# Performance work log

Measured on AMD Instinct MI355X. Metric: run time of the kernel, lower is better.

Reference implementation:

```python
import jax, jax.numpy as jnp
import numpy as np

D = 512
H = 4
HD = D // H
FF = 4 * D
B = 512
T = 128
EMA_K = 128
LOC_K = 4
DECAY = 0.9
STEP = 0.5 / np.sqrt(128 / 32)  # 0.25
EPS = 1e-5


def layernorm(x, g, b):
    mu = jnp.mean(x, axis=-1, keepdims=True)
    var = jnp.mean(jnp.square(x - mu), axis=-1, keepdims=True)
    return (x - mu) * jax.lax.rsqrt(var + EPS) * g + b


def dwconv_causal(x, w):
    # x: (B,T,D), w: (D,K); torch Conv1d(groups=D, padding=K-1) sliced to [:T]
    K = w.shape[1]
    xt = jnp.transpose(x, (0, 2, 1))  # (B,D,T)
    y = jax.lax.conv_general_dilated(
        xt, w[:, None, :], window_strides=(1,), padding=[(K - 1, 0)],
        feature_group_count=x.shape[-1], dimension_numbers=('NCT', 'OIT', 'NCT'))
    return jnp.transpose(y, (0, 2, 1))


def rope(qk, cos, sin):
    # qk: (B,H,T,HD)
    x1, x2 = jnp.split(qk, 2, axis=-1)
    rot = jnp.concatenate([-x2, x1], axis=-1)
    return qk * cos + rot * sin


def setup_inputs() -> dict:
    key = jax.random.key(0)
    ks = jax.random.split(key, 24)
    s = 0.02
    inp = {
        'parallel_repr': jax.random.normal(ks[0], (B, T, D), jnp.float32),
        'sequential_state': jax.random.normal(ks[1], (B, D), jnp.float32),
        'q_w': jax.random.normal(ks[2], (D, D), jnp.float32) * s,
        'q_b': jnp.zeros((D,), jnp.float32),
        'k_w': jax.random.normal(ks[3], (D, D), jnp.float32) * s,
        'k_b': jnp.zeros((D,), jnp.float32),
        'v_w': jax.random.normal(ks[4], (D, D), jnp.float32) * s,
        'v_b': jnp.zeros((D,), jnp.float32),
        'o_w': jax.random.normal(ks[5], (D, D), jnp.float32) * s,
        'o_b': jnp.zeros((D,), jnp.float32),
        'local_w': jax.random.normal(ks[6], (D, LOC_K), jnp.float32) * 0.1,
        'local_b': jax.random.normal(ks[7], (D,), jnp.float32) * 0.1,
        'delta_w': jax.random.normal(ks[8], (3 * D, D), jnp.float32) * s,
        'delta_b': jnp.zeros((D,), jnp.float32),
        'gate_w': jax.random.normal(ks[9], (3 * D, D), jnp.float32) * s,
        'gate_b': jnp.zeros((D,), jnp.float32),
        'dn_g': jnp.ones((D,), jnp.float32), 'dn_b': jnp.zeros((D,), jnp.float32),
        'ln1_g': jnp.ones((D,), jnp.float32), 'ln1_b': jnp.zeros((D,), jnp.float32),
        'ln2_g': jnp.ones((D,), jnp.float32), 'ln2_b': jnp.zeros((D,), jnp.float32),
        'ln3_g': jnp.ones((D,), jnp.float32), 'ln3_b': jnp.zeros((D,), jnp.float32),
        'ln4_g': jnp.ones((D,), jnp.float32), 'ln4_b': jnp.zeros((D,), jnp.float32),
        'seq_w': jax.random.normal(ks[10], (D, D), jnp.float32) * s,
        'seq_b': jnp.zeros((D,), jnp.float32),
        'ffn_w1': jax.random.normal(ks[11], (D, FF), jnp.float32) * s,
        'ffn_b1': jnp.zeros((FF,), jnp.float32),
        'ffn_w2': jax.random.normal(ks[12], (FF, D), jnp.float32) * s,
        'ffn_b2': jnp.zeros((D,), jnp.float32),
    }
    # EMA kernel: coefficient (1-d)*d^lag on x[t-lag]; stored flipped as in torch
    ema = (1.0 - DECAY) * DECAY ** jnp.arange(EMA_K, dtype=jnp.float32)
    inp['ema_w'] = jnp.broadcast_to(ema[::-1][None, :], (D, EMA_K))
    return inp


def reference(parallel_repr, sequential_state, q_w, q_b, k_w, k_b, v_w, v_b,
              o_w, o_b, local_w, local_b, delta_w, delta_b, gate_w, gate_b,
              dn_g, dn_b, ln1_g, ln1_b, ln2_g, ln2_b, ln3_g, ln3_b, ln4_g, ln4_b,
              seq_w, seq_b, ffn_w1, ffn_b1, ffn_w2, ffn_b2, ema_w):
    x = parallel_repr
    Bb, Tt, Dd = x.shape
    # --- RoPE causal attention ---
    inv_freq = 1.0 / (10000.0 ** (jnp.arange(0, HD, 2, dtype=jnp.float32) / HD))
    t = jnp.arange(Tt, dtype=jnp.float32)
    freqs = jnp.outer(t, inv_freq)                      # (T, HD/2)
    emb = jnp.concatenate([freqs, freqs], axis=-1)      # (T, HD)
    cos = jnp.cos(emb)[None, None]
    sin = jnp.sin(emb)[None, None]
    def heads(y):
        return jnp.transpose(y.reshape(Bb, Tt, H, HD), (0, 2, 1, 3))
    q = rope(heads(x @ q_w + q_b), cos, sin)
    k = rope(heads(x @ k_w + k_b), cos, sin)
    v = heads(x @ v_w + v_b)
    scores = jnp.einsum('bhtd,bhsd->bhts', q, k) / np.sqrt(HD)
    causal = jnp.tril(jnp.ones((Tt, Tt), dtype=bool))
    scores = jnp.where(causal, scores, jnp.float32(-1e9))
    attn = jax.nn.softmax(scores, axis=-1)
    attn_out = jnp.einsum('bhts,bhsd->bhtd', attn, v)
    attn_out = jnp.transpose(attn_out, (0, 2, 1, 3)).reshape(Bb, Tt, Dd)
    attn_out = attn_out @ o_w + o_b
    x1 = layernorm(x + attn_out, ln1_g, ln1_b)
    # --- depthwise causal convs ---
    local_hist = dwconv_causal(x1, local_w) + local_b
    global_sum = dwconv_causal(x1, ema_w)
    combined = jnp.concatenate([x1, local_hist, global_sum], axis=-1)  # (B,T,3D)
    deltas = jax.nn.sigmoid(combined @ gate_w + gate_b) * jnp.tanh(combined @ delta_w + delta_b)
    deltas = layernorm(deltas, dn_g, dn_b)
    acc = jnp.cumsum(deltas, axis=1) * STEP
    states = layernorm(sequential_state[:, None, :] + acc, ln3_g, ln3_b)
    seq_guidance = states @ seq_w + seq_b
    ffn_in = x1 + 0.3 * seq_guidance
    h = jax.nn.gelu(ffn_in @ ffn_w1 + ffn_b1, approximate=False)
    ffn_out = h @ ffn_w2 + ffn_b2
    out = layernorm(x1 + ffn_out, ln2_g, ln2_b)
    final_state = layernorm(states[:, -1, :], ln4_g, ln4_b)
    return out, final_state
```

## Files before the change

kernel.cpp:

```cpp
#include <hip/hip_runtime.h>
#include <cstddef>
#include <cstdint>

#define BB   512
#define TT   128
#define DD   512
#define HH   4
#define HDIM 128
#define FFD  2048
#define NROWS (BB * TT)
#define SLOT ((size_t)NROWS * DD)

typedef unsigned short u16;
typedef __bf16 bf16x8 __attribute__((ext_vector_type(8)));
typedef float  f32x4  __attribute__((ext_vector_type(4)));

__device__ __forceinline__ u16 f2b(float x) {
    union { float f; unsigned u; } v; v.f = x;
    unsigned r = v.u + 0x7FFFu + ((v.u >> 16) & 1u);
    return (u16)(r >> 16);
}
__device__ __forceinline__ float b2f(u16 u) {
    union { unsigned u; float f; } v; v.u = (unsigned)u << 16; return v.f;
}
__device__ __forceinline__ float fast_gelu(float v) {
    float t = v * (0.7978845608028654f + 0.0356774081f * v * v);
    float e = __expf(2.f * t);
    float th = 1.f - 2.f / (e + 1.f);
    return 0.5f * v * (1.f + th);
}
__device__ __forceinline__ void glds16(const void* g, void* l) {
    __builtin_amdgcn_global_load_lds(
        (const __attribute__((address_space(1))) void*)g,
        (__attribute__((address_space(3))) void*)l, 16, 0, 0);
}

#define PH_BAR() do { __builtin_amdgcn_sched_barrier(0); \
                      __builtin_amdgcn_s_barrier(); \
                      __builtin_amdgcn_sched_barrier(0); } while (0)

template<int MODE>
__global__ __launch_bounds__(512, 2)
void gemm256(const u16* __restrict__ A, const u16* __restrict__ BT,
             const float* __restrict__ bias, void* __restrict__ Cout, int ldc,
             const float* __restrict__ addsrc, int K, int M)
{
    __shared__ u16 S[65536];
    const int tid = threadIdx.x;
    const int gx  = gridDim.x;
    const int nwg = gx * gridDim.y;
    int orig = blockIdx.y * gx + blockIdx.x;
    orig = (orig & 7) * (nwg >> 3) + (orig >> 3);
    const int row0 = (orig / gx) * 256;
    const int col0 = (orig % gx) * 256;

    const int lane = tid & 63;
    const int wid  = tid >> 6;
    const int wm   = wid >> 2;
    const int wn   = wid & 3;
    const int fr   = lane & 15;
    const int kq   = lane >> 4;

    const int c0 = wid * 128 + lane;
    const int c1 = c0 + 64;
    const int l0 = c0 ^ (((c0 >> 5) & 1) << 1);
    const int l1 = c1 ^ (((c1 >> 5) & 1) << 1);
    const int sr0 = l0 >> 2, sk0 = (l0 & 3) * 8;
    const int sr1 = l1 >> 2, sk1 = (l1 & 3) * 8;
    const u16* ApG = A  + (size_t)row0 * K;
    const u16* BpG = BT + (size_t)col0 * K;

    auto stA = [&](int kt, int kh) {
        char* slot = (char*)S + ((((kt & 1) << 1) + kh) << 14);
        const u16* g = ApG + kt * 64 + kh * 32;
        glds16(g + (size_t)sr0 * K + sk0, slot + c0 * 16);
        glds16(g + (size_t)sr1 * K + sk1, slot + c1 * 16);
    };
    auto stB = [&](int kt, int kh) {
        char* slot = (char*)S + 65536 + ((((kt & 1) << 1) + kh) << 14);
        const u16* g = BpG + kt * 64 + kh * 32;
        glds16(g + (size_t)sr0 * K + sk0, slot + c0 * 16);
        glds16(g + (size_t)sr1 * K + sk1, slot + c1 * 16);
    };
    auto rdA = [&](int p, int kh, int m) -> bf16x8 {
        const int row = wm * 128 + m * 16 + fr;
        const int L = (row * 64 + kq * 16) ^ (((row >> 3) & 1) << 5);
        return *(const bf16x8*)((char*)S + (((p << 1) + kh) << 14) + L);
    };
    auto rdB = [&](int p, int kh, int n) -> bf16x8 {
        const int col = wn * 64 + n * 16 + fr;
        const int L = (col * 64 + kq * 16) ^ (((col >> 3) & 1) << 5);
        return *(const bf16x8*)((char*)S + 65536 + (((p << 1) + kh) << 14) + L);
    };

    f32x4 acc[8][4];
#pragma unroll
    for (int m = 0; m < 8; ++m)
#pragma unroll
        for (int n = 0; n < 4; ++n) acc[m][n] = (f32x4){0.f, 0.f, 0.f, 0.f};

    const int NKT = K >> 6;

    stA(0, 0); stA(0, 1); stB(0, 0); stB(0, 1);
    stB(1, 0); stA(1, 0); stB(1, 1);
    asm volatile("s_waitcnt vmcnt(6)" ::: "memory");
    __builtin_amdgcn_s_barrier();

    bf16x8 b0, b1, b2, b3;
#define MFMA16(MH, A0, A1, A2, A3)                                              \
    do {                                                                        \
        __builtin_amdgcn_s_setprio(1);                                          \
        bf16x8 aa_[4] = {A0, A1, A2, A3};                                       \
        bf16x8 bb_[4] = {b0, b1, b2, b3};                                       \
        _Pragma("unroll")                                                       \
        for (int m_ = 0; m_ < 4; ++m_)                                          \
            _Pragma("unroll")                                                   \
            for (int n_ = 0; n_ < 4; ++n_)                                      \
                acc[(MH) * 4 + m_][n_] = __builtin_amdgcn_mfma_f32_16x16x32_bf16( \
                    aa_[m_], bb_[n_], acc[(MH) * 4 + m_][n_], 0, 0, 0);         \
        __builtin_amdgcn_s_setprio(0);                                          \
    } while (0)

    for (int kt = 0; kt < NKT; ++kt) {
        const int p = kt & 1;
        const bool s1 = (kt + 1 < NKT);
        const bool s2 = (kt + 2 < NKT);
        {
            bf16x8 a0 = rdA(p, 0, 0), a1 = rdA(p, 0, 1), a2 = rdA(p, 0, 2), a3 = rdA(p, 0, 3);
            b0 = rdB(p, 0, 0); b1 = rdB(p, 0, 1); b2 = rdB(p, 0, 2); b3 = rdB(p, 0, 3);
            if (s1) stA(kt + 1, 1);
            PH_BAR();
            MFMA16(0, a0, a1, a2, a3);
            PH_BAR();
        }
        {
            bf16x8 a0 = rdA(p, 0, 4), a1 = rdA(p, 0, 5), a2 = rdA(p, 0, 6), a3 = rdA(p, 0, 7);
            if (s2) stB(kt + 2, 0);
            PH_BAR();
            MFMA16(1, a0, a1, a2, a3);
            PH_BAR();
        }
        {
            bf16x8 a0 = rdA(p, 1, 0), a1 = rdA(p, 1, 1), a2 = rdA(p, 1, 2), a3 = rdA(p, 1, 3);
            b0 = rdB(p, 1, 0); b1 = rdB(p, 1, 1); b2 = rdB(p, 1, 2); b3 = rdB(p, 1, 3);
            if (s2) stA(kt + 2, 0);
            PH_BAR();
            MFMA16(0, a0, a1, a2, a3);
            PH_BAR();
        }
        {
            bf16x8 a0 = rdA(p, 1, 4), a1 = rdA(p, 1, 5), a2 = rdA(p, 1, 6), a3 = rdA(p, 1, 7);
            if (s2) stB(kt + 2, 1);
            PH_BAR();
            MFMA16(1, a0, a1, a2, a3);
            if (s2)      asm volatile("s_waitcnt vmcnt(6)" ::: "memory");
            else if (s1) asm volatile("s_waitcnt vmcnt(0)" ::: "memory");
            PH_BAR();
        }
    }
#undef MFMA16

#pragma unroll
    for (int m = 0; m < 8; ++m) {
#pragma unroll
        for (int jj = 0; jj < 4; ++jj) {
            const int r = row0 + wm * 128 + m * 16 + kq * 4 + jj;
#pragma unroll
            for (int n = 0; n < 4; ++n) {
                const int c = col0 + wn * 64 + n * 16 + fr;
                float v = acc[m][n][jj] + bias[c];
                if constexpr (MODE == 2) {
                    ((u16*)Cout)[(size_t)r * ldc + c] =
                        f2b(addsrc[(size_t)r * M + c] + 0.3f * v);
                } else if constexpr (MODE == 3) {
                    ((u16*)Cout)[(size_t)r * ldc + c] = f2b(fast_gelu(v));
                } else if constexpr (MODE == 6) {
                    float pth = __shfl_xor(v, 1);
                    if ((fr & 1) == 0) {
                        float sg = 1.f / (1.f + __expf(-v));
                        float e  = __expf(2.f * pth);
                        float th = 1.f - 2.f / (e + 1.f);
                        ((u16*)Cout)[(size_t)r * ldc + (c >> 1)] = f2b(sg * th);
                    }
                } else {
                    ((u16*)Cout)[(size_t)r * ldc + c] = f2b(v);
                }
            }
        }
    }
}

template<int MODE>
__global__ __launch_bounds__(256)
void gemm_bf16(const u16* __restrict__ A, const u16* __restrict__ BT,
               const float* __restrict__ bias, void* __restrict__ Cout, int ldc,
               const float* __restrict__ addsrc, void* __restrict__ aux,
               int K, int M)
{
    __shared__ u16 smem[16384];
    const int tid = threadIdx.x;
    const int gx  = gridDim.x;
    const int nwg = gx * gridDim.y;
    int orig = blockIdx.y * gx + blockIdx.x;
    if ((nwg & 7) == 0) orig = (orig & 7) * (nwg >> 3) + (orig >> 3);
    const int row0 = (orig / gx) * 128;
    const int col0 = (orig % gx) * 128;

    const int lane = tid & 63;
    const int w    = tid >> 6;
    const int wr   = (w >> 1) * 64;
    const int wc   = (w & 1) * 64;
    const int fr   = lane & 15;
    const int kg   = (lane >> 4) * 8;

    f32x4 acc[4][4];
#pragma unroll
    for (int m = 0; m < 4; ++m)
#pragma unroll
        for (int n = 0; n < 4; ++n) acc[m][n] = (f32x4){0.f, 0.f, 0.f, 0.f};

    const int srow = tid >> 2;
    const int skb  = (tid & 3) * 8;
    const u16* Ag = A  + (size_t)(row0 + srow) * K + skb;
    const u16* Bg = BT + (size_t)(col0 + srow) * K + skb;
    const int soff = srow * 32 + skb;

    auto stage = [&](int kt, int buf) {
        const int ko = kt * 32;
        u16* as = smem + buf * 8192 + soff;
        u16* bs = smem + buf * 8192 + 4096 + soff;
        glds16(Ag + ko,                  as);
        glds16(Ag + (size_t)64 * K + ko, as + 2048);
        glds16(Bg + ko,                  bs);
        glds16(Bg + (size_t)64 * K + ko, bs + 2048);
    };

    const int nk = K >> 5;
    stage(0, 0);
    for (int k = 0; k < nk; ++k) {
        if (k + 1 < nk) {
            stage(k + 1, (k + 1) & 1);
            asm volatile("s_waitcnt vmcnt(4)" ::: "memory");
        } else {
            asm volatile("s_waitcnt vmcnt(0)" ::: "memory");
        }
        __syncthreads();
        const u16* As = smem + (k & 1) * 8192;
        const u16* Bs = As + 4096;
        bf16x8 af[4], bfr[4];
#pragma unroll
        for (int m = 0; m < 4; ++m)
            af[m] = *reinterpret_cast<const bf16x8*>(&As[(wr + m * 16 + fr) * 32 + kg]);
#pragma unroll
        for (int n = 0; n < 4; ++n)
            bfr[n] = *reinterpret_cast<const bf16x8*>(&Bs[(wc + n * 16 + fr) * 32 + kg]);
#pragma unroll
        for (int m = 0; m < 4; ++m)
#pragma unroll
            for (int n = 0; n < 4; ++n)
                acc[m][n] = __builtin_amdgcn_mfma_f32_16x16x32_bf16(af[m], bfr[n], acc[m][n], 0, 0, 0);
        __syncthreads();
    }

    if constexpr (MODE == 7) {
        if (col0 >= 1024) {
#pragma unroll
            for (int m = 0; m < 4; ++m)
#pragma unroll
                for (int j = 0; j < 4; ++j) {
                    const int tl = wr + m * 16 + (lane >> 4) * 4 + j;
#pragma unroll
                    for (int n = 0; n < 4; ++n) {
                        const int dc = wc + n * 16 + fr;
                        float v = acc[m][n][j] + bias[col0 + dc];
                        *(u16*)((char*)smem + dc * 256 + ((tl * 2) ^ ((dc & 7) << 4))) = f2b(v);
                    }
                }
            __syncthreads();
            u16* dst = (u16*)aux + ((size_t)((row0 >> 7) * 4 + ((col0 - 1024) >> 7)) << 14);
#pragma unroll
            for (int i = 0; i < 8; ++i)
                *(uint4*)(dst + (size_t)(i * 256 + tid) * 8) =
                    *(const uint4*)((char*)smem + (size_t)(i * 256 + tid) * 16);
        } else {
#pragma unroll
            for (int m = 0; m < 4; ++m)
#pragma unroll
                for (int j = 0; j < 4; ++j) {
                    const int r = row0 + wr + m * 16 + (lane >> 4) * 4 + j;
#pragma unroll
                    for (int n = 0; n < 4; ++n) {
                        const int c = col0 + wc + n * 16 + fr;
                        ((u16*)Cout)[(size_t)r * 1024 + c] = f2b(acc[m][n][j] + bias[c]);
                    }
                }
        }
    }
    (void)ldc; (void)addsrc;
}

__global__ __launch_bounds__(256)
void wtrans_kernel(const float* __restrict__ W, u16* __restrict__ WT, int K, int M,
                   int rmul, int roff)
{
    __shared__ float t[32][33];
    const int m0 = blockIdx.x * 32;
    const int k0 = blockIdx.y * 32;
    const int tx = threadIdx.x;
    const int ty = threadIdx.y;
#pragma unroll
    for (int i = 0; i < 4; ++i) {
        int k = ty * 4 + i;
        t[k][tx] = W[(size_t)(k0 + k) * M + m0 + tx];
    }
    __syncthreads();
#pragma unroll
    for (int i = 0; i < 4; ++i) {
        int m = ty * 4 + i;
        WT[(size_t)((m0 + m) * rmul + roff) * K + k0 + tx] = f2b(t[tx][m]);
    }
}

__global__ void cast_f2b_kernel(const float* __restrict__ in, u16* __restrict__ out, size_t n4)
{
    size_t i = (size_t)blockIdx.x * blockDim.x + threadIdx.x;
    if (i >= n4) return;
    float4 v = reinterpret_cast<const float4*>(in)[i];
    union { u16 u[4]; uint2 d; } p;
    p.u[0] = f2b(v.x); p.u[1] = f2b(v.y); p.u[2] = f2b(v.z); p.u[3] = f2b(v.w);
    reinterpret_cast<uint2*>(out)[i] = p.d;
}

__global__ void rope_table_kernel(float* __restrict__ tabc, float* __restrict__ tabs)
{
    int idx = blockIdx.x * blockDim.x + threadIdx.x;
    if (idx >= TT * 64) return;
    int t = idx >> 6, j = idx & 63;
    float invf = expf(-(float)j * (9.210340371976184f / 64.f));
    float ang  = (float)t * invf;
    tabc[idx] = cosf(ang);
    tabs[idx] = sinf(ang);
}

__global__ void bias_build_kernel(const float* qb, const float* kb, const float* vb,
                                  const float* gb, const float* db,
                                  float* qkvb, float* gdb)
{
    int i = blockIdx.x * blockDim.x + threadIdx.x;
    if (i >= 512) return;
    qkvb[i] = qb[i]; qkvb[512 + i] = kb[i]; qkvb[1024 + i] = vb[i];
    gdb[2 * i] = gb[i]; gdb[2 * i + 1] = db[i];
}

__global__ __launch_bounds__(256)
void attn_mfma_kernel(const u16* __restrict__ QKg, const u16* __restrict__ VTg,
                      u16* __restrict__ Og,
                      const float* __restrict__ tabc, const float* __restrict__ tabs)
{
    __shared__ u16 SA[128 * 128];
    __shared__ u16 SB[128 * 128];
    const int h = blockIdx.x, b = blockIdx.y;
    const int tid  = threadIdx.x;
    const int lane = tid & 63;
    const int w    = tid >> 6;
    const int fr   = lane & 15;
    const int kq   = lane >> 4;
    const size_t baseq = ((size_t)(b * TT)) * 1024 + (size_t)h * HDIM;
    const size_t baseo = ((size_t)(b * TT)) * DD + (size_t)h * HDIM;

    {
        const int tg = tid >> 4;
        const int dg = tid & 15;
        const int j0 = (dg & 7) * 8;
        const bool hi = (dg & 8) != 0;
        for (int r = 0; r < 8; ++r) {
            const int t = r * 16 + tg;
            uint4 qv = *(const uint4*)(QKg + baseq + (size_t)t * 1024 + dg * 8);
            uint4 kv = *(const uint4*)(QKg + baseq + 512 + (size_t)t * 1024 + dg * 8);
            unsigned qa[4] = {qv.x, qv.y, qv.z, qv.w};
            unsigned ka[4] = {kv.x, kv.y, kv.z, kv.w};
            unsigned qb[4], kb[4];
#pragma unroll
            for (int i = 0; i < 4; ++i) {
                qb[i] = __shfl_xor((int)qa[i], 8);
                kb[i] = __shfl_xor((int)ka[i], 8);
            }
            const float* cp = tabc + t * 64 + j0;
            const float* sp = tabs + t * 64 + j0;
            u16 oq[8], ok[8];
#pragma unroll
            for (int e = 0; e < 8; ++e) {
                float fq = b2f((u16)(qa[e >> 1] >> ((e & 1) * 16)));
                float gq = b2f((u16)(qb[e >> 1] >> ((e & 1) * 16)));
                float fk = b2f((u16)(ka[e >> 1] >> ((e & 1) * 16)));
                float gk = b2f((u16)(kb[e >> 1] >> ((e & 1) * 16)));
                float c = cp[e], s = sp[e];
                oq[e] = f2b(hi ? fq * c + gq * s : fq * c - gq * s);
                ok[e] = f2b(hi ? fk * c + gk * s : fk * c - gk * s);
            }
            const int cb = (dg * 16) ^ ((t & 7) << 4);
            *(uint4*)((char*)SA + t * 256 + cb) = *(const uint4*)oq;
            *(uint4*)((char*)SB + t * 256 + cb) = *(const uint4*)ok;
        }
    }
    __syncthreads();

    f32x4 acc[2][8];
#pragma unroll
    for (int m = 0; m < 2; ++m)
#pragma unroll
        for (int n = 0; n < 8; ++n) acc[m][n] = (f32x4){0.f, 0.f, 0.f, 0.f};

    for (int k0 = 0; k0 < 128; k0 += 32) {
        const int cb = (k0 + kq * 8) * 2;
        bf16x8 af[2];
#pragma unroll
        for (int m = 0; m < 2; ++m) {
            const int row = w * 32 + m * 16 + fr;
            af[m] = *(const bf16x8*)((char*)SA + row * 256 + (cb ^ ((row & 7) << 4)));
        }
#pragma unroll
        for (int n = 0; n < 8; ++n) {
            const int row = n * 16 + fr;
            bf16x8 bf = *(const bf16x8*)((char*)SB + row * 256 + (cb ^ ((row & 7) << 4)));
            acc[0][n] = __builtin_amdgcn_mfma_f32_16x16x32_bf16(af[0], bf, acc[0][n], 0, 0, 0);
            acc[1][n] = __builtin_amdgcn_mfma_f32_16x16x32_bf16(af[1], bf, acc[1][n], 0, 0, 0);
        }
    }
    __syncthreads();

    {
        const u16* vsrc = VTg + ((size_t)(b * HH + h) << 14);
#pragma unroll
        for (int i = 0; i < 8; ++i)
            glds16(vsrc + (size_t)(i * 256 + tid) * 8,
                   SB + (size_t)(i * 256 + tid) * 8);
    }

    const float SC = 0.08838834764831845f;
#pragma unroll
    for (int m = 0; m < 2; ++m) {
#pragma unroll
        for (int j = 0; j < 4; ++j) {
            const int t = w * 32 + m * 16 + kq * 4 + j;
            float mx = -3.0e38f;
#pragma unroll
            for (int n = 0; n < 8; ++n) {
                const int s = n * 16 + fr;
                float v = acc[m][n][j];
                v = (s <= t) ? v * SC : -3.0e38f;
                acc[m][n][j] = v;
                mx = fmaxf(mx, v);
            }
            mx = fmaxf(mx, __shfl_xor(mx, 1));
            mx = fmaxf(mx, __shfl_xor(mx, 2));
            mx = fmaxf(mx, __shfl_xor(mx, 4));
            mx = fmaxf(mx, __shfl_xor(mx, 8));
            float sum = 0.f;
#pragma unroll
            for (int n = 0; n < 8; ++n) {
                float e = __expf(acc[m][n][j] - mx);
                acc[m][n][j] = e; sum += e;
            }
            sum += __shfl_xor(sum, 1); sum += __shfl_xor(sum, 2);
            sum += __shfl_xor(sum, 4); sum += __shfl_xor(sum, 8);
            const float inv = 1.f / sum;
#pragma unroll
            for (int n = 0; n < 8; ++n) {
                const int s = n * 16 + fr;
                *(u16*)((char*)SA + t * 256 + ((s * 2) ^ ((t & 7) << 4))) =
                    f2b(acc[m][n][j] * inv);
            }
        }
    }
    __syncthreads();

    f32x4 oa[2][8];
#pragma unroll
    for (int m = 0; m < 2; ++m)
#pragma unroll
        for (int n = 0; n < 8; ++n) oa[m][n] = (f32x4){0.f, 0.f, 0.f, 0.f};

    for (int k0 = 0; k0 < 128; k0 += 32) {
        const int cb = (k0 + kq * 8) * 2;
        bf16x8 pa[2];
#pragma unroll
        for (int m = 0; m < 2; ++m) {
            const int row = w * 32 + m * 16 + fr;
            pa[m] = *(const bf16x8*)((char*)SA + row * 256 + (cb ^ ((row & 7) << 4)));
        }
#pragma unroll
        for (int n = 0; n < 8; ++n) {
            const int row = n * 16 + fr;
            bf16x8 vb = *(const bf16x8*)((char*)SB + row * 256 + (cb ^ ((row & 7) << 4)));
            oa[0][n] = __builtin_amdgcn_mfma_f32_16x16x32_bf16(pa[0], vb, oa[0][n], 0, 0, 0);
            oa[1][n] = __builtin_amdgcn_mfma_f32_16x16x32_bf16(pa[1], vb, oa[1][n], 0, 0, 0);
        }
    }

#pragma unroll
    for (int m = 0; m < 2; ++m)
#pragma unroll
        for (int j = 0; j < 4; ++j) {
            const int t = w * 32 + m * 16 + kq * 4 + j;
            u16* orow = Og + baseo + (size_t)t * DD;
#pragma unroll
            for (int n = 0; n < 8; ++n)
                orow[n * 16 + fr] = f2b(oa[m][j * 0 + n][j] * 0.f + oa[m][n][j]);
        }
}

__device__ __forceinline__ float2 blk_red512(float v, float (*red)[2], int tid)
{
    float s = v, ss = v * v;
#pragma unroll
    for (int off = 1; off < 64; off <<= 1) {
        s  += __shfl_xor(s, off);
        ss += __shfl_xor(ss, off);
    }
    if ((tid & 63) == 0) { red[tid >> 6][0] = s; red[tid >> 6][1] = ss; }
    __syncthreads();
    float S = 0.f, SS = 0.f;
#pragma unroll
    for (int w = 0; w < 8; ++w) { S += red[w][0]; SS += red[w][1]; }
    return make_float2(S, SS);
}

__global__ __launch_bounds__(512)
void ln1_chain_kernel(const float* __restrict__ x, const u16* __restrict__ oo,
                      const float* __restrict__ g, const float* __restrict__ bb,
                      const float* __restrict__ lw, const float* __restrict__ lb,
                      float* __restrict__ X1, u16* __restrict__ Cb)
{
    __shared__ float red[2][8][2];
    const int b = blockIdx.x, d = threadIdx.x;
    const float g_ = g[d], b_ = bb[d];
    const float w0 = lw[d * 4 + 0], w1 = lw[d * 4 + 1],
                w2 = lw[d * 4 + 2], w3 = lw[d * 4 + 3];
    const float lb_ = lb[d];
    const size_t rb = (size_t)b * TT;
    float h1 = 0.f, h2 = 0.f, h3 = 0.f, ema = 0.f;
    float v = x[(rb + 0) * DD + d] + b2f(oo[(rb + 0) * DD + d]);
    for (int t = 0; t < TT; ++t) {
        const int tn = (t < TT - 1) ? t + 1 : t;
        float vn = x[(rb + tn) * DD + d] + b2f(oo[(rb + tn) * DD + d]);
        float2 r = blk_red512(v, red[t & 1], d);
        float mu  = r.x * (1.f / DD);
        float var = r.y * (1.f / DD) - mu * mu;
        float x1v = (v - mu) * rsqrtf(var + 1e-5f) * g_ + b_;
        const size_t row = rb + t;
        X1[row * DD + d] = x1v;
        u16* crow = Cb + row * 1536;
        crow[d] = f2b(x1v);
        crow[512 + d]  = f2b(lb_ + w3 * x1v + w2 * h1 + w1 * h2 + w0 * h3);
        ema = 0.9f * ema + 0.1f * x1v;
        crow[1024 + d] = f2b(ema);
        h3 = h2; h2 = h1; h1 = x1v;
        v = vn;
    }
}

__global__ __launch_bounds__(512)
void state_chain_kernel(const u16* __restrict__ deltasB, const float* __restrict__ seqst,
                        const float* __restrict__ dng, const float* __restrict__ dnb,
                        const float* __restrict__ g3, const float* __restrict__ b3,
                        const float* __restrict__ g4, const float* __restrict__ b4,
                        u16* __restrict__ statesb, float* __restrict__ fstate)
{
    __shared__ float red[2][8][2];
    const int b = blockIdx.x, d = threadIdx.x;
    const float gd_ = dng[d], bd_ = dnb[d], g3_ = g3[d], b3_ = b3[d];
    const float seq = seqst[(size_t)b * DD + d];
    const size_t rb = (size_t)b * TT;
    float cum = 0.f;
    float v = b2f(deltasB[(rb + 0) * DD + d]);
    for (int t = 0; t < TT; ++t) {
        const int tn = (t < TT - 1) ? t + 1 : t;
        float vn = b2f(deltasB[(rb + tn) * DD + d]);
        float2 r0 = blk_red512(v, red[0], d);
        float mu  = r0.x * (1.f / DD);
        float var = r0.y * (1.f / DD) - mu * mu;
        float nd  = (v - mu) * rsqrtf(var + 1e-5f) * gd_ + bd_;
        cum += nd;
        float sv = seq + cum * 0.25f;
        float2 r1 = blk_red512(sv, red[1], d);
        mu  = r1.x * (1.f / DD);
        var = r1.y * (1.f / DD) - mu * mu;
        float o = (sv - mu) * rsqrtf(var + 1e-5f) * g3_ + b3_;
        statesb[(rb + t) * DD + d] = f2b(o);
        if (t == TT - 1) {
            float2 r2 = blk_red512(o, red[0], d);
            float mu4  = r2.x * (1.f / DD);
            float var4 = r2.y * (1.f / DD) - mu4 * mu4;
            fstate[(size_t)b * DD + d] = (o - mu4) * rsqrtf(var4 + 1e-5f) * g4[d] + b4[d];
        }
        v = vn;
    }
}

__global__ __launch_bounds__(256)
void ln2_kernel(const float* __restrict__ a, const u16* __restrict__ badd,
                const float* __restrict__ g, const float* __restrict__ bb,
                float* __restrict__ out)
{
    const int row = blockIdx.x;
    const int tid = threadIdx.x;
    const float* ap = a + (size_t)row * DD;
    const u16*   bp = badd + (size_t)row * DD;
    float v0 = ap[tid]       + b2f(bp[tid]);
    float v1 = ap[tid + 256] + b2f(bp[tid + 256]);
    float s  = v0 + v1;
    float ss = v0 * v0 + v1 * v1;
#pragma unroll
    for (int off = 1; off < 64; off <<= 1) {
        s  += __shfl_xor(s, off);
        ss += __shfl_xor(ss, off);
    }
    __shared__ float sm1[4], sm2[4];
    const int wid = tid >> 6;
    if ((tid & 63) == 0) { sm1[wid] = s; sm2[wid] = ss; }
    __syncthreads();
    s  = sm1[0] + sm1[1] + sm1[2] + sm1[3];
    ss = sm2[0] + sm2[1] + sm2[2] + sm2[3];
    const float mu  = s * (1.f / DD);
    const float var = ss * (1.f / DD) - mu * mu;
    const float r   = rsqrtf(var + 1e-5f);
    float* op = out + (size_t)row * DD;
    op[tid]       = (v0 - mu) * r * g[tid]       + bb[tid];
    op[tid + 256] = (v1 - mu) * r * g[tid + 256] + bb[tid + 256];
}

extern "C" void kernel_launch(void* const* d_in, const int* in_sizes, int n_in,
                              void* d_out, int out_size, void* d_ws, size_t ws_size,
                              hipStream_t stream)
{
    const float* x       = (const float*)d_in[0];
    const float* seqst   = (const float*)d_in[1];
    const float* q_w     = (const float*)d_in[2];
    const float* q_b     = (const float*)d_in[3];
    const float* k_w     = (const float*)d_in[4];
    const float* k_b     = (const float*)d_in[5];
    const float* v_w     = (const float*)d_in[6];
    const float* v_b     = (const float*)d_in[7];
    const float* o_w     = (const float*)d_in[8];
    const float* o_b     = (const float*)d_in[9];
    const float* local_w = (const float*)d_in[10];
    const float* local_b = (const float*)d_in[11];
    const float* delta_w = (const float*)d_in[12];
    const float* delta_b = (const float*)d_in[13];
    const float* gate_w  = (const float*)d_in[14];
    const float* gate_b  = (const float*)d_in[15];
    const float* dn_g    = (const float*)d_in[16];
    const float* dn_b    = (const float*)d_in[17];
    const float* ln1_g   = (const float*)d_in[18];
    const float* ln1_b   = (const float*)d_in[19];
    const float* ln2_g   = (const float*)d_in[20];
    const float* ln2_b   = (const float*)d_in[21];
    const float* ln3_g   = (const float*)d_in[22];
    const float* ln3_b   = (const float*)d_in[23];
    const float* ln4_g   = (const float*)d_in[24];
    const float* ln4_b   = (const float*)d_in[25];
    const float* seq_w   = (const float*)d_in[26];
    const float* seq_b   = (const float*)d_in[27];
    const float* ffn_w1  = (const float*)d_in[28];
    const float* ffn_b1  = (const float*)d_in[29];
    const float* ffn_w2  = (const float*)d_in[30];
    const float* ffn_b2  = (const float*)d_in[31];
    (void)in_sizes; (void)n_in; (void)out_size; (void)ws_size;

    float* out = (float*)d_out;
    char*  ws  = (char*)d_ws;
    const size_t MB = (size_t)1 << 20;

    u16*   xb      = (u16*)(ws + 0);
    u16*   QKb     = (u16*)(ws + 64 * MB);
    u16*   VTb     = (u16*)(ws + 192 * MB);
    u16*   attnb   = (u16*)(ws + 256 * MB);
    u16*   Oob     = (u16*)(ws + 0);
    u16*   Cb      = (u16*)(ws + 64 * MB);
    u16*   deltasB = (u16*)(ws + 256 * MB);
    u16*   statesb = (u16*)(ws + 320 * MB);
    u16*   ffn_inb = (u16*)(ws + 0);
    u16*   hb      = (u16*)(ws + 64 * MB);
    u16*   Fob     = (u16*)(ws + 320 * MB);
    u16*   WSq  = (u16*)(ws + 448 * MB);
    u16*   WSo  = (u16*)(ws + 450 * MB);
    u16*   WSgd = (u16*)(ws + 451 * MB);
    u16*   WSs  = (u16*)(ws + 455 * MB);
    u16*   WSf1 = (u16*)(ws + 456 * MB);
    u16*   WSf2 = (u16*)(ws + 458 * MB);
    float* qkvb = (float*)(ws + 460 * MB);
    float* gdb  = (float*)(ws + 461 * MB);

    float* X1     = out;
    float* tabc   = out + SLOT;
    float* tabs   = tabc + TT * 64;
    float* fstate = out + SLOT;

    const size_t NE = (size_t)NROWS * DD;

    rope_table_kernel<<<(TT * 64 + 255) / 256, 256, 0, stream>>>(tabc, tabs);
    cast_f2b_kernel<<<(unsigned)((NE / 4 + 255) / 256), 256, 0, stream>>>(x, xb, NE / 4);
    bias_build_kernel<<<2, 256, 0, stream>>>(q_b, k_b, v_b, gate_b, delta_b, qkvb, gdb);
    auto wt = [&](const float* W, u16* WT, int K, int M, int rmul, int roff) {
        wtrans_kernel<<<dim3(M / 32, K / 32), dim3(32, 8), 0, stream>>>(W, WT, K, M, rmul, roff);
    };
    wt(q_w, WSq, DD, DD, 1, 0);
    wt(k_w, WSq + (size_t)512 * DD, DD, DD, 1, 0);
    wt(v_w, WSq + (size_t)1024 * DD, DD, DD, 1, 0);
    wt(o_w, WSo, DD, DD, 1, 0);
    wt(gate_w,  WSgd, 3 * DD, DD, 2, 0);
    wt(delta_w, WSgd, 3 * DD, DD, 2, 1);
    wt(seq_w, WSs, DD, DD, 1, 0);
    wt(ffn_w1, WSf1, DD, FFD, 1, 0);
    wt(ffn_w2, WSf2, FFD, DD, 1, 0);

    gemm_bf16<7><<<dim3(12, 512), 256, 0, stream>>>(
        xb, WSq, qkvb, QKb, 1024, nullptr, VTb, DD, 1536);

    attn_mfma_kernel<<<dim3(HH, BB), 256, 0, stream>>>(QKb, VTb, attnb, tabc, tabs);

    gemm256<4><<<dim3(2, 256), 512, 0, stream>>>(
        attnb, WSo, o_b, Oob, DD, nullptr, DD, DD);

    ln1_chain_kernel<<<BB, 512, 0, stream>>>(x, Oob, ln1_g, ln1_b, local_w, local_b, X1, Cb);

    gemm256<6><<<dim3(4, 256), 512, 0, stream>>>(
        Cb, WSgd, gdb, deltasB, DD, nullptr, 3 * DD, 1024);

    state_chain_kernel<<<BB, 512, 0, stream>>>(
        deltasB, seqst, dn_g, dn_b, ln3_g, ln3_b, ln4_g, ln4_b, statesb, fstate);

    gemm256<2><<<dim3(2, 256), 512, 0, stream>>>(
        statesb, WSs, seq_b, ffn_inb, DD, X1, DD, DD);

    gemm256<3><<<dim3(8, 256), 512, 0, stream>>>(
        ffn_inb, WSf1, ffn_b1, hb, FFD, nullptr, DD, FFD);
    gemm256<4><<<dim3(2, 256), 512, 0, stream>>>(
        hb, WSf2, ffn_b2, Fob, DD, nullptr, FFD, DD);

    ln2_kernel<<<NROWS, 256, 0, stream>>>(X1, Fob, ln2_g, ln2_b, out);
}
```

Baseline: 1.668 ms.

## Reschedule GEMM main loop into N-half phases with fewer scheduling barriers

After: 1.655 ms. About the same (-0.8%).

```diff
diff --git a/kernel.cpp b/kernel.cpp
--- a/kernel.cpp
+++ b/kernel.cpp
@@ -35,9 +35,9 @@
         (__attribute__((address_space(3))) void*)l, 16, 0, 0);
 }
 
-#define PH_BAR() do { __builtin_amdgcn_sched_barrier(0); \
-                      __builtin_amdgcn_s_barrier(); \
-                      __builtin_amdgcn_sched_barrier(0); } while (0)
+#define BAR() asm volatile("s_barrier" ::: "memory")
+#define MM(ACC, AV, BV) \
+    ACC = __builtin_amdgcn_mfma_f32_16x16x32_bf16(AV, BV, ACC, 0, 0, 0)
 
 template<int MODE>
 __global__ __launch_bounds__(512, 2)
@@ -102,63 +102,81 @@
     const int NKT = K >> 6;
 
     stA(0, 0); stA(0, 1); stB(0, 0); stB(0, 1);
-    stB(1, 0); stA(1, 0); stB(1, 1);
+    stB(1, 0); stB(1, 1); stA(1, 0);
     asm volatile("s_waitcnt vmcnt(6)" ::: "memory");
-    __builtin_amdgcn_s_barrier();
-
-    bf16x8 b0, b1, b2, b3;
-#define MFMA16(MH, A0, A1, A2, A3)                                              \
-    do {                                                                        \
-        __builtin_amdgcn_s_setprio(1);                                          \
-        bf16x8 aa_[4] = {A0, A1, A2, A3};                                       \
-        bf16x8 bb_[4] = {b0, b1, b2, b3};                                       \
-        _Pragma("unroll")                                                       \
-        for (int m_ = 0; m_ < 4; ++m_)                                          \
-            _Pragma("unroll")                                                   \
-            for (int n_ = 0; n_ < 4; ++n_)                                      \
-                acc[(MH) * 4 + m_][n_] = __builtin_amdgcn_mfma_f32_16x16x32_bf16( \
-                    aa_[m_], bb_[n_], acc[(MH) * 4 + m_][n_], 0, 0, 0);         \
-        __builtin_amdgcn_s_setprio(0);                                          \
-    } while (0)
+    BAR();
 
     for (int kt = 0; kt < NKT; ++kt) {
         const int p = kt & 1;
         const bool s1 = (kt + 1 < NKT);
         const bool s2 = (kt + 2 < NKT);
-        {
-            bf16x8 a0 = rdA(p, 0, 0), a1 = rdA(p, 0, 1), a2 = rdA(p, 0, 2), a3 = rdA(p, 0, 3);
-            b0 = rdB(p, 0, 0); b1 = rdB(p, 0, 1); b2 = rdB(p, 0, 2); b3 = rdB(p, 0, 3);
-            if (s1) stA(kt + 1, 1);
-            PH_BAR();
-            MFMA16(0, a0, a1, a2, a3);
-            PH_BAR();
-        }
-        {
-            bf16x8 a0 = rdA(p, 0, 4), a1 = rdA(p, 0, 5), a2 = rdA(p, 0, 6), a3 = rdA(p, 0, 7);
-            if (s2) stB(kt + 2, 0);
-            PH_BAR();
-            MFMA16(1, a0, a1, a2, a3);
-            PH_BAR();
-        }
-        {
-            bf16x8 a0 = rdA(p, 1, 0), a1 = rdA(p, 1, 1), a2 = rdA(p, 1, 2), a3 = rdA(p, 1, 3);
-            b0 = rdB(p, 1, 0); b1 = rdB(p, 1, 1); b2 = rdB(p, 1, 2); b3 = rdB(p, 1, 3);
-            if (s2) stA(kt + 2, 0);
-            PH_BAR();
-            MFMA16(0, a0, a1, a2, a3);
-            PH_BAR();
-        }
-        {
-            bf16x8 a0 = rdA(p, 1, 4), a1 = rdA(p, 1, 5), a2 = rdA(p, 1, 6), a3 = rdA(p, 1, 7);
-            if (s2) stB(kt + 2, 1);
-            PH_BAR();
-            MFMA16(1, a0, a1, a2, a3);
-            if (s2)      asm volatile("s_waitcnt vmcnt(6)" ::: "memory");
-            else if (s1) asm volatile("s_waitcnt vmcnt(0)" ::: "memory");
-            PH_BAR();
-        }
-    }
-#undef MFMA16
+        bf16x8 a0, a1, a2, a3, a4, a5, a6, a7;
+        bf16x8 b00, b01, b02, b03, b10, b11, b12, b13;
+
+        if (s1) stA(kt + 1, 1);
+        a0 = rdA(p, 0, 0); a1 = rdA(p, 0, 1); a2 = rdA(p, 0, 2); a3 = rdA(p, 0, 3);
+        a4 = rdA(p, 1, 0); a5 = rdA(p, 1, 1); a6 = rdA(p, 1, 2); a7 = rdA(p, 1, 3);
+        b00 = rdB(p, 0, 0); b01 = rdB(p, 0, 1);
+        b10 = rdB(p, 1, 0); b11 = rdB(p, 1, 1);
+        BAR();
+        __builtin_amdgcn_s_setprio(1);
+        MM(acc[0][0], a0, b00); MM(acc[0][1], a0, b01);
+        MM(acc[1][0], a1, b00); MM(acc[1][1], a1, b01);
+        MM(acc[2][0], a2, b00); MM(acc[2][1], a2, b01);
+        MM(acc[3][0], a3, b00); MM(acc[3][1], a3, b01);
+        MM(acc[0][0], a4, b10); MM(acc[0][1], a4, b11);
+        MM(acc[1][0], a5, b10); MM(acc[1][1], a5, b11);
+        MM(acc[2][0], a6, b10); MM(acc[2][1], a6, b11);
+        MM(acc[3][0], a7, b10); MM(acc[3][1], a7, b11);
+        __builtin_amdgcn_s_setprio(0);
+        BAR();
+
+        b02 = rdB(p, 0, 2); b03 = rdB(p, 0, 3);
+        b12 = rdB(p, 1, 2); b13 = rdB(p, 1, 3);
+        BAR();
+        __builtin_amdgcn_s_setprio(1);
+        MM(acc[0][2], a0, b02); MM(acc[0][3], a0, b03);
+        MM(acc[1][2], a1, b02); MM(acc[1][3], a1, b03);
+        MM(acc[2][2], a2, b02); MM(acc[2][3], a2, b03);
+        MM(acc[3][2], a3, b02); MM(acc[3][3], a3, b03);
+        MM(acc[0][2], a4, b12); MM(acc[0][3], a4, b13);
+        MM(acc[1][2], a5, b12); MM(acc[1][3], a5, b13);
+        MM(acc[2][2], a6, b12); MM(acc[2][3], a6, b13);
+        MM(acc[3][2], a7, b12); MM(acc[3][3], a7, b13);
+        __builtin_amdgcn_s_setprio(0);
+        BAR();
+
+        if (s2) stB(kt + 2, 0);
+        a0 = rdA(p, 0, 4); a1 = rdA(p, 0, 5); a2 = rdA(p, 0, 6); a3 = rdA(p, 0, 7);
+        a4 = rdA(p, 1, 4); a5 = rdA(p, 1, 5); a6 = rdA(p, 1, 6); a7 = rdA(p, 1, 7);
+        BAR();
+        __builtin_amdgcn_s_setprio(1);
+        MM(acc[4][0], a0, b00); MM(acc[4][1], a0, b01);
+        MM(acc[5][0], a1, b00); MM(acc[5][1], a1, b01);
+        MM(acc[6][0], a2, b00); MM(acc[6][1], a2, b01);
+        MM(acc[7][0], a3, b00); MM(acc[7][1], a3, b01);
+        MM(acc[4][0], a4, b10); MM(acc[4][1], a4, b11);
+        MM(acc[5][0], a5, b10); MM(acc[5][1], a5, b11);
+        MM(acc[6][0], a6, b10); MM(acc[6][1], a6, b11);
+        MM(acc[7][0], a7, b10); MM(acc[7][1], a7, b11);
+        __builtin_amdgcn_s_setprio(0);
+        BAR();
+
+        if (s2) { stB(kt + 2, 1); stA(kt + 2, 0); }
+        __builtin_amdgcn_s_setprio(1);
+        MM(acc[4][2], a0, b02); MM(acc[4][3], a0, b03);
+        MM(acc[5][2], a1, b02); MM(acc[5][3], a1, b03);
+        MM(acc[6][2], a2, b02); MM(acc[6][3], a2, b03);
+        MM(acc[7][2], a3, b02); MM(acc[7][3], a3, b03);
+        MM(acc[4][2], a4, b12); MM(acc[4][3], a4, b13);
+        MM(acc[5][2], a5, b12); MM(acc[5][3], a5, b13);
+        MM(acc[6][2], a6, b12); MM(acc[6][3], a6, b13);
+        MM(acc[7][2], a7, b12); MM(acc[7][3], a7, b13);
+        __builtin_amdgcn_s_setprio(0);
+        if (s2)      asm volatile("s_waitcnt vmcnt(6)" ::: "memory");
+        else if (s1) asm volatile("s_waitcnt vmcnt(0)" ::: "memory");
+        if (s1) BAR();
+    }
 
 #pragma unroll
     for (int m = 0; m < 8; ++m) {
@@ -506,7 +524,7 @@
             u16* orow = Og + baseo + (size_t)t * DD;
 #pragma unroll
             for (int n = 0; n < 8; ++n)
-                orow[n * 16 + fr] = f2b(oa[m][j * 0 + n][j] * 0.f + oa[m][n][j]);
+                orow[n * 16 + fr] = f2b(oa[m][n][j]);
         }
 }
 
```

## Software-pipeline LDS fragment reads ahead of MFMA clusters in GEMM main loop

Applied to the files above, without the earlier changes.

Result: no change. 1.667 ms (-0.1%).

```diff
diff --git a/kernel.cpp b/kernel.cpp
--- a/kernel.cpp
+++ b/kernel.cpp
@@ -35,9 +35,10 @@
         (__attribute__((address_space(3))) void*)l, 16, 0, 0);
 }
 
-#define PH_BAR() do { __builtin_amdgcn_sched_barrier(0); \
-                      __builtin_amdgcn_s_barrier(); \
-                      __builtin_amdgcn_sched_barrier(0); } while (0)
+#define BAR() asm volatile("s_barrier" ::: "memory")
+#define SB0() __builtin_amdgcn_sched_barrier(0)
+#define MM(ACC, AV, BV) \
+    ACC = __builtin_amdgcn_mfma_f32_16x16x32_bf16(AV, BV, ACC, 0, 0, 0)
 
 template<int MODE>
 __global__ __launch_bounds__(512, 2)
@@ -101,64 +102,80 @@
 
     const int NKT = K >> 6;
 
-    stA(0, 0); stA(0, 1); stB(0, 0); stB(0, 1);
-    stB(1, 0); stA(1, 0); stB(1, 1);
-    asm volatile("s_waitcnt vmcnt(6)" ::: "memory");
-    __builtin_amdgcn_s_barrier();
-
-    bf16x8 b0, b1, b2, b3;
-#define MFMA16(MH, A0, A1, A2, A3)                                              \
-    do {                                                                        \
-        __builtin_amdgcn_s_setprio(1);                                          \
-        bf16x8 aa_[4] = {A0, A1, A2, A3};                                       \
-        bf16x8 bb_[4] = {b0, b1, b2, b3};                                       \
-        _Pragma("unroll")                                                       \
-        for (int m_ = 0; m_ < 4; ++m_)                                          \
-            _Pragma("unroll")                                                   \
-            for (int n_ = 0; n_ < 4; ++n_)                                      \
-                acc[(MH) * 4 + m_][n_] = __builtin_amdgcn_mfma_f32_16x16x32_bf16( \
-                    aa_[m_], bb_[n_], acc[(MH) * 4 + m_][n_], 0, 0, 0);         \
-        __builtin_amdgcn_s_setprio(0);                                          \
+    stA(0, 0); stB(0, 0); stA(0, 1); stB(0, 1);
+    stA(1, 0); stB(1, 0); stB(1, 1);
+    asm volatile("s_waitcnt vmcnt(10)" ::: "memory");
+    BAR();
+    bf16x8 aC0, aC1, aC2, aC3, aN0, aN1, aN2, aN3;
+    bf16x8 bC0, bC1, bC2, bC3, bN0, bN1, bN2, bN3;
+    aC0 = rdA(0, 0, 0); aC1 = rdA(0, 0, 1); aC2 = rdA(0, 0, 2); aC3 = rdA(0, 0, 3);
+    bC0 = rdB(0, 0, 0); bC1 = rdB(0, 0, 1); bC2 = rdB(0, 0, 2); bC3 = rdB(0, 0, 3);
+
+#define CLUSTER(R, A0_, A1_, A2_, A3_, B0_, B1_, B2_, B3_)                    \
+    do {                                                                      \
+        __builtin_amdgcn_s_setprio(1);                                        \
+        MM(acc[(R)+0][0], A0_, B0_); MM(acc[(R)+0][1], A0_, B1_);             \
+        MM(acc[(R)+0][2], A0_, B2_); MM(acc[(R)+0][3], A0_, B3_);             \
+        MM(acc[(R)+1][0], A1_, B0_); MM(acc[(R)+1][1], A1_, B1_);             \
+        MM(acc[(R)+1][2], A1_, B2_); MM(acc[(R)+1][3], A1_, B3_);             \
+        MM(acc[(R)+2][0], A2_, B0_); MM(acc[(R)+2][1], A2_, B1_);             \
+        MM(acc[(R)+2][2], A2_, B2_); MM(acc[(R)+2][3], A2_, B3_);             \
+        MM(acc[(R)+3][0], A3_, B0_); MM(acc[(R)+3][1], A3_, B1_);             \
+        MM(acc[(R)+3][2], A3_, B2_); MM(acc[(R)+3][3], A3_, B3_);             \
+        __builtin_amdgcn_s_setprio(0);                                        \
     } while (0)
 
     for (int kt = 0; kt < NKT; ++kt) {
         const int p = kt & 1;
         const bool s1 = (kt + 1 < NKT);
         const bool s2 = (kt + 2 < NKT);
-        {
-            bf16x8 a0 = rdA(p, 0, 0), a1 = rdA(p, 0, 1), a2 = rdA(p, 0, 2), a3 = rdA(p, 0, 3);
-            b0 = rdB(p, 0, 0); b1 = rdB(p, 0, 1); b2 = rdB(p, 0, 2); b3 = rdB(p, 0, 3);
-            if (s1) stA(kt + 1, 1);
-            PH_BAR();
-            MFMA16(0, a0, a1, a2, a3);
-            PH_BAR();
-        }
-        {
-            bf16x8 a0 = rdA(p, 0, 4), a1 = rdA(p, 0, 5), a2 = rdA(p, 0, 6), a3 = rdA(p, 0, 7);
-            if (s2) stB(kt + 2, 0);
-            PH_BAR();
-            MFMA16(1, a0, a1, a2, a3);
-            PH_BAR();
-        }
-        {
-            bf16x8 a0 = rdA(p, 1, 0), a1 = rdA(p, 1, 1), a2 = rdA(p, 1, 2), a3 = rdA(p, 1, 3);
-            b0 = rdB(p, 1, 0); b1 = rdB(p, 1, 1); b2 = rdB(p, 1, 2); b3 = rdB(p, 1, 3);
-            if (s2) stA(kt + 2, 0);
-            PH_BAR();
-            MFMA16(0, a0, a1, a2, a3);
-            PH_BAR();
-        }
-        {
-            bf16x8 a0 = rdA(p, 1, 4), a1 = rdA(p, 1, 5), a2 = rdA(p, 1, 6), a3 = rdA(p, 1, 7);
-            if (s2) stB(kt + 2, 1);
-            PH_BAR();
-            MFMA16(1, a0, a1, a2, a3);
-            if (s2)      asm volatile("s_waitcnt vmcnt(6)" ::: "memory");
-            else if (s1) asm volatile("s_waitcnt vmcnt(0)" ::: "memory");
-            PH_BAR();
-        }
-    }
-#undef MFMA16
+
+        BAR();
+        if (s1) stA(kt + 1, 1);
+        aN0 = rdA(p, 0, 4); aN1 = rdA(p, 0, 5); aN2 = rdA(p, 0, 6); aN3 = rdA(p, 0, 7);
+        asm volatile("s_waitcnt lgkmcnt(4)" ::: "memory");
+        SB0();
+        CLUSTER(0, aC0, aC1, aC2, aC3, bC0, bC1, bC2, bC3);
+
+        BAR();
+        if (s2) {
+            stB(kt + 2, 0);
+            asm volatile("s_waitcnt vmcnt(10)" ::: "memory");
+        } else {
+            asm volatile("s_waitcnt vmcnt(0)" ::: "memory");
+        }
+        aC0 = rdA(p, 1, 0); aC1 = rdA(p, 1, 1); aC2 = rdA(p, 1, 2); aC3 = rdA(p, 1, 3);
+        bN0 = rdB(p, 1, 0); bN1 = rdB(p, 1, 1); bN2 = rdB(p, 1, 2); bN3 = rdB(p, 1, 3);
+        asm volatile("s_waitcnt lgkmcnt(8)" ::: "memory");
+        SB0();
+        CLUSTER(4, aN0, aN1, aN2, aN3, bC0, bC1, bC2, bC3);
+
+        BAR();
+        if (s2) stA(kt + 2, 0);
+        aN0 = rdA(p, 1, 4); aN1 = rdA(p, 1, 5); aN2 = rdA(p, 1, 6); aN3 = rdA(p, 1, 7);
+        asm volatile("s_waitcnt lgkmcnt(4)" ::: "memory");
+        SB0();
+        CLUSTER(0, aC0, aC1, aC2, aC3, bN0, bN1, bN2, bN3);
+
+        BAR();
+        if (s2) {
+            stB(kt + 2, 1);
+            asm volatile("s_waitcnt vmcnt(8)" ::: "memory");
+        } else {
+            asm volatile("s_waitcnt vmcnt(0)" ::: "memory");
+        }
+        if (s1) {
+            const int pn = p ^ 1;
+            aC0 = rdA(pn, 0, 0); aC1 = rdA(pn, 0, 1); aC2 = rdA(pn, 0, 2); aC3 = rdA(pn, 0, 3);
+            bC0 = rdB(pn, 0, 0); bC1 = rdB(pn, 0, 1); bC2 = rdB(pn, 0, 2); bC3 = rdB(pn, 0, 3);
+            asm volatile("s_waitcnt lgkmcnt(8)" ::: "memory");
+        } else {
+            asm volatile("s_waitcnt lgkmcnt(0)" ::: "memory");
+        }
+        SB0();
+        CLUSTER(4, aN0, aN1, aN2, aN3, bN0, bN1, bN2, bN3);
+    }
+#undef CLUSTER
 
 #pragma unroll
     for (int m = 0; m < 8; ++m) {
@@ -506,7 +523,7 @@
             u16* orow = Og + baseo + (size_t)t * DD;
 #pragma unroll
             for (int n = 0; n < 8; ++n)
-                orow[n * 16 + fr] = f2b(oa[m][j * 0 + n][j] * 0.f + oa[m][n][j]);
+                orow[n * 16 + fr] = f2b(oa[m][n][j]);
         }
 }
 
```
